# Optimization experiments

Hardware: AMD Instinct MI355X
Metric: run time of the kernel (lower is better)

## Reference

```python
import jax, jax.numpy as jnp
import numpy as np

B, T, E, H = 8, 2048, 256, 8
D = E // H  # head_size = 32
EPS = 1e-5  # torch LayerNorm default


def _layernorm(x, g, b):
    m = jnp.mean(x, axis=-1, keepdims=True)
    v = jnp.var(x, axis=-1, keepdims=True)
    return (x - m) / jnp.sqrt(v + EPS) * g + b


def setup_inputs() -> dict:
    key = jax.random.key(0)
    ks = jax.random.split(key, 9)
    s = lambda k, shape, fan: (jax.random.normal(k, shape, jnp.float32) / np.sqrt(fan)).astype(jnp.float32)
    return {
        "x": jax.random.normal(ks[0], (B, T, E), jnp.float32),
        "wq": s(ks[1], (H, E, D), E),
        "wk": s(ks[2], (H, E, D), E),
        "wv": s(ks[3], (H, E, D), E),
        "w_lin": s(ks[4], (E, E), E),
        "b_lin": jnp.zeros((E,), jnp.float32),
        "g1": jnp.ones((E,), jnp.float32),
        "beta1": jnp.zeros((E,), jnp.float32),
        "g2": jnp.ones((E,), jnp.float32),
        "beta2": jnp.zeros((E,), jnp.float32),
        "w_f1": s(ks[5], (E, 4 * E), E),
        "b_f1": jnp.zeros((4 * E,), jnp.float32),
        "w_f2": s(ks[6], (4 * E, E), 4 * E),
        "b_f2": jnp.zeros((E,), jnp.float32),
    }


def reference(x, wq, wk, wv, w_lin, b_lin, g1, beta1, g2, beta2, w_f1, b_f1, w_f2, b_f2):
    b, t, e = x.shape
    xn = _layernorm(x, g1, beta1)  # norm1
    # all heads at once: (B,T,E) x (H,E,D) -> (B,H,T,D)
    q = jnp.einsum('bte,hed->bhtd', xn, wq)
    k = jnp.einsum('bte,hed->bhtd', xn, wk)
    v = jnp.einsum('bte,hed->bhtd', xn, wv)
    # scale uses C = embedding_size (as in source, not head_size)
    scores = jnp.einsum('bhtd,bhsd->bhts', q, k) * (e ** -0.5)
    mask = jnp.tril(jnp.ones((t, t), bool))  # (query t, key s)
    scores = jnp.where(mask[None, None, :, :], scores, -jnp.inf)
    # source applies softmax over dim=1 of (B,T,T) = the QUERY axis -> axis 2 of bhts
    attn = jax.nn.softmax(scores, axis=2)
    heads = jnp.einsum('bhts,bhsd->bhtd', attn, v)
    heads = heads.transpose(0, 2, 1, 3).reshape(b, t, e)  # concat over heads
    xh = xn + heads  # residual around attention
    xl = xh @ w_lin + b_lin  # projection (dropout is identity at eval)
    x2 = _layernorm(xl, g2, beta2)  # norm2
    ff = jax.nn.relu(x2 @ w_f1 + b_f1) @ w_f2 + b_f2  # FFN (dropout identity)
    return x2 + ff
```

## Files before the change

### kernel.cpp

```cpp
#include <hip/hip_runtime.h>
#include <math.h>

#define TT 2048
#define TE 256
#define NTOK 16384
#define QSCALE (0.0625f * 1.44269504088896f)

typedef short  bf16x8 __attribute__((ext_vector_type(8)));
typedef float  f32x4  __attribute__((ext_vector_type(4)));
typedef float  f32x16 __attribute__((ext_vector_type(16)));
typedef unsigned short u16x4 __attribute__((ext_vector_type(4)));
typedef unsigned short u16x8 __attribute__((ext_vector_type(8)));

__device__ __forceinline__ unsigned short f2b(float f) {
    union { float f; unsigned int u; } v; v.f = f;
    unsigned int r = v.u + 0x7FFF + ((v.u >> 16) & 1);
    return (unsigned short)(r >> 16);
}
__device__ __forceinline__ float b2f(unsigned short u) {
    union { unsigned int i; float f; } v; v.i = ((unsigned int)u) << 16;
    return v.f;
}
#if __has_builtin(__builtin_amdgcn_cvt_pk_bf16_f32)
__device__ __forceinline__ unsigned int pk_bf16(float a, float b) {
    typedef __bf16 bf2 __attribute__((ext_vector_type(2)));
    union { bf2 v; unsigned int u; } u;
    u.v = __builtin_amdgcn_cvt_pk_bf16_f32(a, b);
    return u.u;
}
#else
__device__ __forceinline__ unsigned int pk_bf16(float a, float b) {
    return (unsigned int)f2b(a) | ((unsigned int)f2b(b) << 16);
}
#endif
#if __has_builtin(__builtin_amdgcn_exp2f)
#define FEXP2(x) __builtin_amdgcn_exp2f(x)
#else
#define FEXP2(x) __expf(0.69314718056f * (x))
#endif
__device__ __forceinline__ void pswap(unsigned &a, unsigned &b) {
#if __has_builtin(__builtin_amdgcn_permlane32_swap)
    auto r = __builtin_amdgcn_permlane32_swap(a, b, false, false);
    a = r[0]; b = r[1];
#else
    asm("v_permlane32_swap_b32 %0, %1" : "+v"(a), "+v"(b));
#endif
}
__device__ __forceinline__ bf16x8 ld8(const unsigned short* p) {
    return *(const bf16x8*)p;
}
__device__ __forceinline__ void gl_lds16(const unsigned short* g, unsigned short* l) {
    __builtin_amdgcn_global_load_lds(
        (const __attribute__((address_space(1))) unsigned int*)(uintptr_t)g,
        (__attribute__((address_space(3))) unsigned int*)(uintptr_t)l,
        16, 0, 0);
}
#define MFMA16(a, b, c) __builtin_amdgcn_mfma_f32_16x16x32_bf16((a), (b), (c), 0, 0, 0)
#define MFMA32(a, b, c) __builtin_amdgcn_mfma_f32_32x32x16_bf16((a), (b), (c), 0, 0, 0)
#define SETPRIO(n) __builtin_amdgcn_s_setprio(n)


__device__ __forceinline__ void soft_pv(const f32x16 st, bf16x8 vv0, bf16x8 vv1,
                                        bool diag, int hi, int l31, f32x16& acc) {
    unsigned Wd[8];
    if (diag) {
#pragma unroll
        for (int j = 0; j < 8; ++j) {
            int r0 = 2 * j;
            int s0 = (r0 & 3) + 8 * (r0 >> 2) + 4 * hi;
            float e0 = (s0 <= l31)     ? FEXP2(st[r0])     : 0.f;
            float e1 = (s0 + 1 <= l31) ? FEXP2(st[r0 + 1]) : 0.f;
            Wd[j] = pk_bf16(e0, e1);
        }
    } else {
#pragma unroll
        for (int j = 0; j < 8; ++j)
            Wd[j] = pk_bf16(FEXP2(st[2 * j]), FEXP2(st[2 * j + 1]));
    }
    pswap(Wd[0], Wd[2]); pswap(Wd[1], Wd[3]);
    pswap(Wd[4], Wd[6]); pswap(Wd[5], Wd[7]);
    union { unsigned u4[4]; bf16x8 v; } pa0, pa1;
    pa0.u4[0] = Wd[0]; pa0.u4[1] = Wd[1]; pa0.u4[2] = Wd[2]; pa0.u4[3] = Wd[3];
    pa1.u4[0] = Wd[4]; pa1.u4[1] = Wd[5]; pa1.u4[2] = Wd[6]; pa1.u4[3] = Wd[7];
    SETPRIO(1);
    acc = MFMA32(pa0.v, vv0, acc);
    acc = MFMA32(pa1.v, vv1, acc);
    SETPRIO(0);
}

__device__ __forceinline__ void accum_exp(const f32x16 st, bool diag,
                                          int hi, int l31, float* acc) {
    if (diag) {
#pragma unroll
        for (int r = 0; r < 16; ++r) {
            int s_local = (r & 3) + 8 * (r >> 2) + 4 * hi;
            acc[r] += (l31 >= s_local) ? FEXP2(st[r]) : 0.f;
        }
    } else {
#pragma unroll
        for (int r = 0; r < 16; ++r) acc[r] += FEXP2(st[r]);
    }
}

__global__ __launch_bounds__(256) void prep(const float* __restrict__ wq,
                                            const float* __restrict__ wk,
                                            const float* __restrict__ wv,
                                            const float* __restrict__ w_lin,
                                            const float* __restrict__ w_f1,
                                            const float* __restrict__ w_f2,
                                            unsigned short* __restrict__ Wqkv,
                                            unsigned short* __restrict__ Wlin,
                                            unsigned short* __restrict__ Wf1,
                                            unsigned short* __restrict__ Wf2,
                                            const float* __restrict__ X,
                                            const float* __restrict__ g,
                                            const float* __restrict__ bta,
                                            unsigned short* __restrict__ Yb) {
    int bid = blockIdx.x;
    if (bid >= 240) {
        int row = (bid - 240) * 4 + (threadIdx.x >> 6);
        int lane = threadIdx.x & 63;
        const float4 v = *(const float4*)&X[(size_t)row * TE + lane * 4];
        float s = v.x + v.y + v.z + v.w;
        float s2 = v.x * v.x + v.y * v.y + v.z * v.z + v.w * v.w;
#pragma unroll
        for (int off = 1; off <= 32; off <<= 1) {
            s  += __shfl_xor(s,  off, 64);
            s2 += __shfl_xor(s2, off, 64);
        }
        float mean = s * (1.0f / TE);
        float var = s2 * (1.0f / TE) - mean * mean;
        float rstd = rsqrtf(var + 1e-5f);
        const float4 gg = *(const float4*)&g[lane * 4];
        const float4 bb = *(const float4*)&bta[lane * 4];
        u16x4 ob = { f2b((v.x - mean) * rstd * gg.x + bb.x),
                     f2b((v.y - mean) * rstd * gg.y + bb.y),
                     f2b((v.z - mean) * rstd * gg.z + bb.z),
                     f2b((v.w - mean) * rstd * gg.w + bb.w) };
        *(u16x4*)&Yb[(size_t)row * TE + lane * 4] = ob;
        return;
    }
    __shared__ unsigned short Tt[64][65];
    int t = threadIdx.x;
    if (bid < 96) {
        int which = bid / 32, h = (bid >> 2) & 7, kt = bid & 3;
        const float* src = ((which == 0) ? wq : (which == 1) ? wk : wv)
                           + (size_t)h * 256 * 32;
        int d = t & 31, kr = t >> 5;
#pragma unroll
        for (int r = 0; r < 8; ++r) {
            int kl = kr * 8 + r;
            Tt[kl][d] = f2b(src[(size_t)(kt * 64 + kl) * 32 + d]);
        }
        __syncthreads();
        int kl = t & 63, dr = t >> 6;
#pragma unroll
        for (int r = 0; r < 8; ++r) {
            int dl = dr * 8 + r;
            Wqkv[(size_t)(which * 256 + h * 32 + dl) * 256 + kt * 64 + kl] = Tt[kl][dl];
        }
        return;
    }
    const float* src; unsigned short* dst; int ldn, ldk, kt, nt;
    if (bid < 112)      { int b2 = bid - 96;  src = w_lin; dst = Wlin; ldn = 256;  ldk = 256;  kt = b2 & 3;  nt = b2 >> 2; }
    else if (bid < 176) { int b3 = bid - 112; src = w_f1;  dst = Wf1;  ldn = 1024; ldk = 256;  kt = b3 >> 4; nt = b3 & 15; }
    else                { int b4 = bid - 176; src = w_f2;  dst = Wf2;  ldn = 256;  ldk = 1024; kt = b4 >> 2; nt = b4 & 3; }
    int n = t & 63, kr = t >> 6;
#pragma unroll
    for (int r = 0; r < 16; ++r) {
        int kl = kr * 16 + r;
        Tt[kl][n] = f2b(src[(size_t)(kt * 64 + kl) * ldn + nt * 64 + n]);
    }
    __syncthreads();
    int klane = t & 63, nr = t >> 6;
#pragma unroll
    for (int r = 0; r < 16; ++r) {
        int nl = nr * 16 + r;
        dst[(size_t)(nt * 64 + nl) * ldk + kt * 64 + klane] = Tt[klane][nl];
    }
}

__global__ __launch_bounds__(256) void ln2_red(const float* __restrict__ Pp,
                                               const float* __restrict__ bias,
                                               const float* __restrict__ g,
                                               const float* __restrict__ bta,
                                               unsigned short* __restrict__ Yb) {
    int row = blockIdx.x * 4 + (threadIdx.x >> 6);
    int lane = threadIdx.x & 63;
    size_t base = (size_t)row * TE + lane * 4;
    const float4 p0 = *(const float4*)&Pp[base];
    const float4 bl = *(const float4*)&bias[lane * 4];
    float4 v;
    v.x = p0.x + bl.x; v.y = p0.y + bl.y;
    v.z = p0.z + bl.z; v.w = p0.w + bl.w;
    float s = v.x + v.y + v.z + v.w;
    float s2 = v.x * v.x + v.y * v.y + v.z * v.z + v.w * v.w;
#pragma unroll
    for (int off = 1; off <= 32; off <<= 1) {
        s  += __shfl_xor(s,  off, 64);
        s2 += __shfl_xor(s2, off, 64);
    }
    float mean = s * (1.0f / TE);
    float var = s2 * (1.0f / TE) - mean * mean;
    float rstd = rsqrtf(var + 1e-5f);
    const float4 gg = *(const float4*)&g[lane * 4];
    const float4 bb = *(const float4*)&bta[lane * 4];
    u16x4 ob = { f2b((v.x - mean) * rstd * gg.x + bb.x),
                 f2b((v.y - mean) * rstd * gg.y + bb.y),
                 f2b((v.z - mean) * rstd * gg.z + bb.z),
                 f2b((v.w - mean) * rstd * gg.w + bb.w) };
    *(u16x4*)&Yb[base] = ob;
}

template<int KS>
__global__ __launch_bounds__(256) void gemm_lds(const unsigned short* __restrict__ A,
                                                int lda,
                                                const unsigned short* __restrict__ Bt,
                                                int ldb,
                                                const float* __restrict__ bias,
                                                const unsigned short* __restrict__ resid,
                                                float* __restrict__ outF,
                                                unsigned short* __restrict__ outB,
                                                int N, int relu) {
    __shared__ unsigned short LDSb[3 * 2048 + 3 * 4096];
    unsigned short* Al = LDSb;
    unsigned short* Bl = LDSb + 3 * 2048;
    int tid = threadIdx.x;
    int w = tid >> 6, lane = tid & 63, q = lane >> 4, col = lane & 15;
    int wm = w & 1, wn = w >> 1;
    int m0 = blockIdx.x * 64;
    int n0 = blockIdx.y * 128;
    f32x4 acc[2][4] = {};
    int srow = lane >> 2;
    int skq  = ((lane & 3) ^ ((srow >> 1) & 3)) * 8;
    const unsigned short* Ag0 = A  + (size_t)(m0 + w * 16 + srow) * lda + skq;
    const unsigned short* Bg0 = Bt + (size_t)(n0 + w * 32 + srow) * ldb + skq;
    const unsigned short* Bg1 = Bg0 + (size_t)16 * ldb;
    int rq = (q ^ ((col >> 1) & 3)) * 8;
#define G_STAGE(bf, kk) do { \
        gl_lds16(Ag0 + (kk), &Al[(bf) * 2048 + (w * 16) * 32]); \
        gl_lds16(Bg0 + (kk), &Bl[(bf) * 4096 + (w * 32) * 32]); \
        gl_lds16(Bg1 + (kk), &Bl[(bf) * 4096 + (w * 32 + 16) * 32]); \
    } while (0)
    G_STAGE(0, 0);
    G_STAGE(1, 32);
#pragma unroll
    for (int k0 = 0; k0 < KS; k0 += 32) {
        const int jb = (k0 >> 5) % 3;
        if (k0 + 32 < KS) { asm volatile("s_waitcnt vmcnt(3)" ::: "memory"); }
        else              { asm volatile("s_waitcnt vmcnt(0)" ::: "memory"); }
        __builtin_amdgcn_s_barrier();
        if (k0 + 64 < KS) G_STAGE((jb + 2) % 3, k0 + 64);
        bf16x8 a[2], b[4];
#pragma unroll
        for (int i = 0; i < 2; ++i)
            a[i] = ld8(&Al[jb * 2048 + (wm * 32 + i * 16 + col) * 32 + rq]);
#pragma unroll
        for (int j = 0; j < 4; ++j)
            b[j] = ld8(&Bl[jb * 4096 + (wn * 64 + j * 16 + col) * 32 + rq]);
#pragma unroll
        for (int i = 0; i < 2; ++i)
#pragma unroll
            for (int j = 0; j < 4; ++j)
                acc[i][j] = MFMA16(a[i], b[j], acc[i][j]);
        __builtin_amdgcn_sched_barrier(0);
    }
#undef G_STAGE
    float* Cb = (float*)LDSb;
    const int CLD = 132;
#pragma unroll
    for (int i = 0; i < 2; ++i) {
        __syncthreads();
#pragma unroll
        for (int j = 0; j < 4; ++j)
#pragma unroll
            for (int r = 0; r < 4; ++r)
                Cb[(wm * 16 + q * 4 + r) * CLD + wn * 64 + j * 16 + col] = acc[i][j][r];
        __syncthreads();
        int row = tid >> 3;
        int seg = (tid & 7) * 16;
        int mloc = (row & 15) + i * 16 + (row >> 4) * 32;
        int m = m0 + mloc;
        int n = n0 + seg;
        float vbuf[16];
#pragma unroll
        for (int u = 0; u < 16; ++u) vbuf[u] = Cb[row * CLD + seg + u];
        if (bias) {
#pragma unroll
            for (int u4 = 0; u4 < 4; ++u4) {
                float4 bb = *(const float4*)&bias[n + u4 * 4];
                vbuf[u4 * 4 + 0] += bb.x; vbuf[u4 * 4 + 1] += bb.y;
                vbuf[u4 * 4 + 2] += bb.z; vbuf[u4 * 4 + 3] += bb.w;
            }
        }
        if (resid) {
            u16x8 r0 = *(const u16x8*)&resid[(size_t)m * N + n];
            u16x8 r1 = *(const u16x8*)&resid[(size_t)m * N + n + 8];
#pragma unroll
            for (int u = 0; u < 8; ++u) {
                vbuf[u]     += b2f(r0[u]);
                vbuf[8 + u] += b2f(r1[u]);
            }
        }
        if (relu) {
#pragma unroll
            for (int u = 0; u < 16; ++u) vbuf[u] = fmaxf(vbuf[u], 0.f);
        }
        if (outF) {
#pragma unroll
            for (int u = 0; u < 16; u += 4)
                *(float4*)&outF[(size_t)m * N + n + u] = *(const float4*)&vbuf[u];
        }
        if (outB) {
            u16x8 o0, o1;
#pragma unroll
            for (int u = 0; u < 8; ++u) { o0[u] = f2b(vbuf[u]); o1[u] = f2b(vbuf[8 + u]); }
            *(u16x8*)&outB[(size_t)m * N + n] = o0;
            *(u16x8*)&outB[(size_t)m * N + n + 8] = o1;
        }
    }
}

__global__ __launch_bounds__(256) void gemm_qkv(const unsigned short* __restrict__ A,
                                                const unsigned short* __restrict__ Bt,
                                                unsigned short* __restrict__ Qd,
                                                unsigned short* __restrict__ Kd,
                                                unsigned short* __restrict__ Vc) {
    const int K = 256;
    __shared__ unsigned short LDSb[3 * 2048 + 3 * 4096];
    unsigned short* Al = LDSb;
    unsigned short* Bl = LDSb + 3 * 2048;
    int tid = threadIdx.x;
    int w = tid >> 6, lane = tid & 63, q = lane >> 4, col = lane & 15;
    int wm = w & 1, wn = w >> 1;
    int m0 = blockIdx.x * 64;
    int n0 = blockIdx.y * 128;
    f32x4 acc[2][4] = {};
    int srow = lane >> 2;
    int skq  = ((lane & 3) ^ ((srow >> 1) & 3)) * 8;
    const unsigned short* Ag0 = A  + (size_t)(m0 + w * 16 + srow) * K + skq;
    const unsigned short* Bg0 = Bt + (size_t)(n0 + w * 32 + srow) * K + skq;
    const unsigned short* Bg1 = Bg0 + (size_t)16 * K;
    int rq = (q ^ ((col >> 1) & 3)) * 8;
#define G_STAGE(bf, kk) do { \
        gl_lds16(Ag0 + (kk), &Al[(bf) * 2048 + (w * 16) * 32]); \
        gl_lds16(Bg0 + (kk), &Bl[(bf) * 4096 + (w * 32) * 32]); \
        gl_lds16(Bg1 + (kk), &Bl[(bf) * 4096 + (w * 32 + 16) * 32]); \
    } while (0)
    G_STAGE(0, 0);
    G_STAGE(1, 32);
#pragma unroll
    for (int k0 = 0; k0 < K; k0 += 32) {
        const int jb = (k0 >> 5) % 3;
        if (k0 + 32 < K) { asm volatile("s_waitcnt vmcnt(3)" ::: "memory"); }
        else             { asm volatile("s_waitcnt vmcnt(0)" ::: "memory"); }
        __builtin_amdgcn_s_barrier();
        if (k0 + 64 < K) G_STAGE((jb + 2) % 3, k0 + 64);
        bf16x8 a[2], b[4];
#pragma unroll
        for (int i = 0; i < 2; ++i)
            a[i] = ld8(&Al[jb * 2048 + (wm * 32 + i * 16 + col) * 32 + rq]);
#pragma unroll
        for (int j = 0; j < 4; ++j)
            b[j] = ld8(&Bl[jb * 4096 + (wn * 64 + j * 16 + col) * 32 + rq]);
#pragma unroll
        for (int i = 0; i < 2; ++i)
#pragma unroll
            for (int j = 0; j < 4; ++j)
                acc[i][j] = MFMA16(a[i], b[j], acc[i][j]);
        __builtin_amdgcn_sched_barrier(0);
    }
#undef G_STAGE
#pragma unroll
    for (int i = 0; i < 2; ++i)
#pragma unroll
    for (int j = 0; j < 4; ++j) {
        int n = n0 + wn * 64 + j * 16 + col;
        int which = n >> 8, h = (n >> 5) & 7, d = n & 31;
        int m = m0 + wm * 32 + i * 16 + q * 4;
        int b = m >> 11, t = m & 2047;
        int bh = b * 8 + h;
        if (which == 0) {
            size_t qb = ((size_t)(bh * 2 + (d >> 4)) * TT + t) * 16 + (d & 15);
#pragma unroll
            for (int r = 0; r < 4; ++r)
                Qd[qb + r * 16] = f2b(acc[i][j][r] * QSCALE);
        } else if (which == 1) {
            size_t kb = ((size_t)(bh * 2 + (d >> 4)) * TT + t) * 16 + (d & 15);
#pragma unroll
            for (int r = 0; r < 4; ++r)
                Kd[kb + r * 16] = f2b(acc[i][j][r]);
        } else {
            uint2 pv;
            pv.x = pk_bf16(acc[i][j][0], acc[i][j][1]);
            pv.y = pk_bf16(acc[i][j][2], acc[i][j][3]);
            *(uint2*)&Vc[(((size_t)bh * 256 + (t >> 3)) * 32 + d) * 8 + (t & 7)] = pv;
        }
    }
}

__global__ __launch_bounds__(256, 2) void attn_cols(const unsigned short* __restrict__ Qd,
                                                    const unsigned short* __restrict__ Kd,
                                                    unsigned short* __restrict__ Vc) {
    __shared__ float Lb[4][32];
    __shared__ float Linv[32];
    int tid = threadIdx.x;
    int w = tid >> 6, lane = tid & 63, hi = lane >> 5, l31 = lane & 31;
    int bh = blockIdx.x;
    int stile = blockIdx.y;
    const unsigned short* Qb = Qd + ((size_t)bh * 2 * TT + l31) * 16 + hi * 8;
    const unsigned short* Kb = Kd + ((size_t)bh * 2 * TT + l31) * 16 + hi * 8;
    const f32x16 z16 = {};
    int sbase = stile * 32;
    bf16x8 a0 = ld8(Kb + (size_t)sbase * 16);
    bf16x8 a1 = ld8(Kb + ((size_t)TT + sbase) * 16);
    float acc[16] = {};
    int c = stile + w;
    bool diagP = (w == 0);
    bf16x8 qP0, qP1, qQ0, qQ1;
    if (c < 64) {
        qP0 = ld8(Qb + (size_t)(c * 32) * 16);
        qP1 = ld8(Qb + ((size_t)TT + c * 32) * 16);
    }
    if (c + 4 < 64) {
        qQ0 = ld8(Qb + (size_t)((c + 4) * 32) * 16);
        qQ1 = ld8(Qb + ((size_t)TT + (c + 4) * 32) * 16);
    }
    while (c + 8 < 64) {
        SETPRIO(1);
        f32x16 stP = MFMA32(a0, qP0, z16); stP = MFMA32(a1, qP1, stP);
        SETPRIO(0);
        qP0 = ld8(Qb + (size_t)((c + 8) * 32) * 16);
        qP1 = ld8(Qb + ((size_t)TT + (c + 8) * 32) * 16);
        SETPRIO(1);
        f32x16 stQ = MFMA32(a0, qQ0, z16); stQ = MFMA32(a1, qQ1, stQ);
        SETPRIO(0);
        accum_exp(stP, diagP, hi, l31, acc); diagP = false;
        if (c + 12 < 64) {
            qQ0 = ld8(Qb + (size_t)((c + 12) * 32) * 16);
            qQ1 = ld8(Qb + ((size_t)TT + (c + 12) * 32) * 16);
        }
        accum_exp(stQ, false, hi, l31, acc);
        c += 8;
    }
    if (c < 64) {
        f32x16 stP = MFMA32(a0, qP0, z16); stP = MFMA32(a1, qP1, stP);
        accum_exp(stP, diagP, hi, l31, acc);
    }
    if (c + 4 < 64) {
        f32x16 stQ = MFMA32(a0, qQ0, z16); stQ = MFMA32(a1, qQ1, stQ);
        accum_exp(stQ, false, hi, l31, acc);
    }
#pragma unroll
    for (int off = 1; off <= 16; off <<= 1)
#pragma unroll
        for (int r = 0; r < 16; ++r) acc[r] += __shfl_xor(acc[r], off, 64);
    if (l31 == 0) {
#pragma unroll
        for (int r = 0; r < 16; ++r) {
            int s_local = (r & 3) + 8 * (r >> 2) + 4 * hi;
            Lb[w][s_local] = acc[r];
        }
    }
    __syncthreads();
    if (tid < 32)
        Linv[tid] = 1.0f / (Lb[0][tid] + Lb[1][tid] + Lb[2][tid] + Lb[3][tid]);
    __syncthreads();
    if (tid < 128) {
        int sbl = tid >> 5;
        int d = tid & 31;
        size_t base = (((size_t)bh * 256 + stile * 4 + sbl) * 32 + d) * 8;
        u16x8 v = *(const u16x8*)&Vc[base];
        u16x8 o;
#pragma unroll
        for (int e = 0; e < 8; ++e) o[e] = f2b(b2f(v[e]) * Linv[sbl * 8 + e]);
        *(u16x8*)&Vc[base] = o;
    }
}

__global__ __launch_bounds__(256, 2) void attn_out(const unsigned short* __restrict__ Qd,
                                                   const unsigned short* __restrict__ Kd,
                                                   const unsigned short* __restrict__ Vc,
                                                   const unsigned short* __restrict__ xnb,
                                                   unsigned short* __restrict__ xh_bf) {
    __shared__ float Ob[4][16][36];
    int tid = threadIdx.x;
    int w = tid >> 6, lane = tid & 63, hi = lane >> 5, l31 = lane & 31;
    int bh = blockIdx.x, b = bh >> 3, h = bh & 7;
    int tt = blockIdx.y;
    const unsigned short* Kb = Kd + ((size_t)bh * 2 * TT + l31) * 16 + hi * 8;
    const unsigned short* Vb = Vc + (size_t)bh * 65536 + hi * 256 + l31 * 8;
    const unsigned short* Qbase = Qd + ((size_t)bh * 2 * TT + l31) * 16 + hi * 8;
    const f32x16 z16 = {};

    int tbase = tt * 32;
    bf16x8 q0 = ld8(Qbase + (size_t)tbase * 16);
    bf16x8 q1 = ld8(Qbase + ((size_t)TT + tbase) * 16);
    f32x16 acc = z16;

    int c = w;
    bf16x8 kP0, kP1, vP0, vP1, kQ0, kQ1, vQ0, vQ1;
    if (c <= tt) {
        kP0 = ld8(Kb + (size_t)c * 512);
        kP1 = ld8(Kb + (size_t)TT * 16 + (size_t)c * 512);
        vP0 = ld8(Vb + (size_t)c * 1024);
        vP1 = ld8(Vb + (size_t)c * 1024 + 512);
    }
    if (c + 4 <= tt) {
        kQ0 = ld8(Kb + (size_t)(c + 4) * 512);
        kQ1 = ld8(Kb + (size_t)TT * 16 + (size_t)(c + 4) * 512);
        vQ0 = ld8(Vb + (size_t)(c + 4) * 1024);
        vQ1 = ld8(Vb + (size_t)(c + 4) * 1024 + 512);
    }
    while (c + 8 <= tt) {
        SETPRIO(1);
        f32x16 stP = MFMA32(kP0, q0, z16); stP = MFMA32(kP1, q1, stP);
        SETPRIO(0);
        kP0 = ld8(Kb + (size_t)(c + 8) * 512);
        kP1 = ld8(Kb + (size_t)TT * 16 + (size_t)(c + 8) * 512);
        SETPRIO(1);
        f32x16 stQ = MFMA32(kQ0, q0, z16); stQ = MFMA32(kQ1, q1, stQ);
        SETPRIO(0);
        soft_pv(stP, vP0, vP1, false, hi, l31, acc);
        vP0 = ld8(Vb + (size_t)(c + 8) * 1024);
        vP1 = ld8(Vb + (size_t)(c + 8) * 1024 + 512);
        if (c + 12 <= tt) {
            kQ0 = ld8(Kb + (size_t)(c + 12) * 512);
            kQ1 = ld8(Kb + (size_t)TT * 16 + (size_t)(c + 12) * 512);
        }
        soft_pv(stQ, vQ0, vQ1, false, hi, l31, acc);
        if (c + 12 <= tt) {
            vQ0 = ld8(Vb + (size_t)(c + 12) * 1024);
            vQ1 = ld8(Vb + (size_t)(c + 12) * 1024 + 512);
        }
        c += 8;
    }
    if (c <= tt) {
        f32x16 stP = MFMA32(kP0, q0, z16); stP = MFMA32(kP1, q1, stP);
        soft_pv(stP, vP0, vP1, c == tt, hi, l31, acc);
    }
    if (c + 4 <= tt) {
        f32x16 stQ = MFMA32(kQ0, q0, z16); stQ = MFMA32(kQ1, q1, stQ);
        soft_pv(stQ, vQ0, vQ1, c + 4 == tt, hi, l31, acc);
    }

#pragma unroll
    for (int half = 0; half < 2; ++half) {
#pragma unroll
        for (int rr = 0; rr < 8; ++rr) {
            int r = half * 8 + rr;
            int t16 = (r & 3) + 8 * ((r >> 2) & 1) + 4 * hi;
            Ob[w][t16][l31] = acc[r];
        }
        __syncthreads();
        if (tid < 128) {
            int row = tid >> 3;
            int c4 = (tid & 7) * 4;
            float4 s0 = *(const float4*)&Ob[0][row][c4];
            float4 s1 = *(const float4*)&Ob[1][row][c4];
            float4 s2 = *(const float4*)&Ob[2][row][c4];
            float4 s3 = *(const float4*)&Ob[3][row][c4];
            size_t base = ((size_t)(b * TT) + tbase + half * 16 + row) * TE
                          + h * 32 + c4;
            u16x4 xv = *(const u16x4*)&xnb[base];
            u16x4 ob = { f2b(s0.x + s1.x + s2.x + s3.x + b2f(xv[0])),
                         f2b(s0.y + s1.y + s2.y + s3.y + b2f(xv[1])),
                         f2b(s0.z + s1.z + s2.z + s3.z + b2f(xv[2])),
                         f2b(s0.w + s1.w + s2.w + s3.w + b2f(xv[3])) };
            *(u16x4*)&xh_bf[base] = ob;
        }
        __syncthreads();
    }
}

extern "C" void kernel_launch(void* const* d_in, const int* in_sizes, int n_in,
                              void* d_out, int out_size, void* d_ws, size_t ws_size,
                              hipStream_t stream) {
    (void)in_sizes; (void)n_in; (void)out_size; (void)ws_size;
    const float* x     = (const float*)d_in[0];
    const float* wq    = (const float*)d_in[1];
    const float* wk    = (const float*)d_in[2];
    const float* wv    = (const float*)d_in[3];
    const float* w_lin = (const float*)d_in[4];
    const float* b_lin = (const float*)d_in[5];
    const float* g1    = (const float*)d_in[6];
    const float* beta1 = (const float*)d_in[7];
    const float* g2    = (const float*)d_in[8];
    const float* beta2 = (const float*)d_in[9];
    const float* w_f1  = (const float*)d_in[10];
    const float* b_f1  = (const float*)d_in[11];
    const float* w_f2  = (const float*)d_in[12];
    const float* b_f2  = (const float*)d_in[13];
    float* out = (float*)d_out;

    char* ws = (char*)d_ws;
    unsigned short* Wqkv_t = (unsigned short*)(ws + 0);
    unsigned short* Wlin_t = (unsigned short*)(ws + 393216);
    unsigned short* Wf1_t  = (unsigned short*)(ws + 524288);
    unsigned short* Wf2_t  = (unsigned short*)(ws + 1048576);
    unsigned short* xn_bf  = (unsigned short*)(ws + 2097152);
    unsigned short* Qbf    = (unsigned short*)(ws + 10485760);
    unsigned short* Kbf    = (unsigned short*)(ws + 18874368);
    unsigned short* Vt     = (unsigned short*)(ws + 27262976);
    unsigned short* xh_bf  = (unsigned short*)(ws + 35651584);
    float*          Pp     = (float*)(ws + 44040192);
    unsigned short* x2_bf  = xn_bf;
    unsigned short* h_bf   = Qbf;

    prep<<<4336, 256, 0, stream>>>(wq, wk, wv, w_lin, w_f1, w_f2,
                                   Wqkv_t, Wlin_t, Wf1_t, Wf2_t,
                                   x, g1, beta1, xn_bf);
    gemm_qkv<<<dim3(256, 6), 256, 0, stream>>>(xn_bf, Wqkv_t, Qbf, Kbf, Vt);
    attn_cols<<<dim3(64, 64), 256, 0, stream>>>(Qbf, Kbf, Vt);
    attn_out<<<dim3(64, 64), 256, 0, stream>>>(Qbf, Kbf, Vt, xn_bf, xh_bf);
    gemm_lds<256><<<dim3(256, 2), 256, 0, stream>>>(xh_bf, 256, Wlin_t, 256,
                                                    nullptr, nullptr, Pp, nullptr, 256, 0);
    ln2_red<<<4096, 256, 0, stream>>>(Pp, b_lin, g2, beta2, x2_bf);
    gemm_lds<256><<<dim3(256, 8), 256, 0, stream>>>(x2_bf, 256, Wf1_t, 256,
                                                    b_f1, nullptr, nullptr, h_bf, 1024, 1);
    gemm_lds<1024><<<dim3(256, 2), 256, 0, stream>>>(h_bf, 1024, Wf2_t, 1024,
                                                     b_f2, x2_bf, out, nullptr, 256, 0);
}
```

Measured before the change: 222.4 us.

## Give each wave its own attention tile instead of splitting keys across waves

Both attention kernels now assign each of the four waves its own 32-row tile (tile = blockIdx.y + 16*w) and let it walk the full causal range alone. Previously four waves split one tile's chunks and reduced through shared memory with block barriers. The cross-wave reduction and __syncthreads are gone, the grid shrinks to 64x16 blocks, and launch bounds rise to 4 blocks per CU. Pairing tiles y and y+16, y+32, y+48 in one block balances the causal triangle's work somewhat, but waves within a block still finish at different times, which risks idle waves and tail imbalance.

```diff
diff --git a/kernel.cpp b/kernel.cpp
--- a/kernel.cpp
+++ b/kernel.cpp
@@ -399,15 +399,14 @@
     }
 }
 
-__global__ __launch_bounds__(256, 2) void attn_cols(const unsigned short* __restrict__ Qd,
+__global__ __launch_bounds__(256, 4) void attn_cols(const unsigned short* __restrict__ Qd,
                                                     const unsigned short* __restrict__ Kd,
                                                     unsigned short* __restrict__ Vc) {
-    __shared__ float Lb[4][32];
-    __shared__ float Linv[32];
+    __shared__ float Lw[4][32];
     int tid = threadIdx.x;
     int w = tid >> 6, lane = tid & 63, hi = lane >> 5, l31 = lane & 31;
     int bh = blockIdx.x;
-    int stile = blockIdx.y;
+    int stile = blockIdx.y + 16 * w;
     const unsigned short* Qb = Qd + ((size_t)bh * 2 * TT + l31) * 16 + hi * 8;
     const unsigned short* Kb = Kd + ((size_t)bh * 2 * TT + l31) * 16 + hi * 8;
     const f32x16 z16 = {};
@@ -415,39 +414,37 @@
     bf16x8 a0 = ld8(Kb + (size_t)sbase * 16);
     bf16x8 a1 = ld8(Kb + ((size_t)TT + sbase) * 16);
     float acc[16] = {};
-    int c = stile + w;
-    bool diagP = (w == 0);
+    int c = stile;
+    bool diagP = true;
     bf16x8 qP0, qP1, qQ0, qQ1;
-    if (c < 64) {
-        qP0 = ld8(Qb + (size_t)(c * 32) * 16);
-        qP1 = ld8(Qb + ((size_t)TT + c * 32) * 16);
-    }
-    if (c + 4 < 64) {
-        qQ0 = ld8(Qb + (size_t)((c + 4) * 32) * 16);
-        qQ1 = ld8(Qb + ((size_t)TT + (c + 4) * 32) * 16);
-    }
-    while (c + 8 < 64) {
+    qP0 = ld8(Qb + (size_t)(c * 32) * 16);
+    qP1 = ld8(Qb + ((size_t)TT + c * 32) * 16);
+    if (c + 1 < 64) {
+        qQ0 = ld8(Qb + (size_t)((c + 1) * 32) * 16);
+        qQ1 = ld8(Qb + ((size_t)TT + (c + 1) * 32) * 16);
+    }
+    while (c + 2 < 64) {
         SETPRIO(1);
         f32x16 stP = MFMA32(a0, qP0, z16); stP = MFMA32(a1, qP1, stP);
         SETPRIO(0);
-        qP0 = ld8(Qb + (size_t)((c + 8) * 32) * 16);
-        qP1 = ld8(Qb + ((size_t)TT + (c + 8) * 32) * 16);
+        qP0 = ld8(Qb + (size_t)((c + 2) * 32) * 16);
+        qP1 = ld8(Qb + ((size_t)TT + (c + 2) * 32) * 16);
         SETPRIO(1);
         f32x16 stQ = MFMA32(a0, qQ0, z16); stQ = MFMA32(a1, qQ1, stQ);
         SETPRIO(0);
         accum_exp(stP, diagP, hi, l31, acc); diagP = false;
-        if (c + 12 < 64) {
-            qQ0 = ld8(Qb + (size_t)((c + 12) * 32) * 16);
-            qQ1 = ld8(Qb + ((size_t)TT + (c + 12) * 32) * 16);
+        if (c + 3 < 64) {
+            qQ0 = ld8(Qb + (size_t)((c + 3) * 32) * 16);
+            qQ1 = ld8(Qb + ((size_t)TT + (c + 3) * 32) * 16);
         }
         accum_exp(stQ, false, hi, l31, acc);
-        c += 8;
+        c += 2;
     }
     if (c < 64) {
         f32x16 stP = MFMA32(a0, qP0, z16); stP = MFMA32(a1, qP1, stP);
         accum_exp(stP, diagP, hi, l31, acc);
     }
-    if (c + 4 < 64) {
+    if (c + 1 < 64) {
         f32x16 stQ = MFMA32(a0, qQ0, z16); stQ = MFMA32(a1, qQ1, stQ);
         accum_exp(stQ, false, hi, l31, acc);
     }
@@ -459,35 +456,38 @@
 #pragma unroll
         for (int r = 0; r < 16; ++r) {
             int s_local = (r & 3) + 8 * (r >> 2) + 4 * hi;
-            Lb[w][s_local] = acc[r];
-        }
-    }
-    __syncthreads();
-    if (tid < 32)
-        Linv[tid] = 1.0f / (Lb[0][tid] + Lb[1][tid] + Lb[2][tid] + Lb[3][tid]);
-    __syncthreads();
-    if (tid < 128) {
-        int sbl = tid >> 5;
-        int d = tid & 31;
+            Lw[w][s_local] = acc[r];
+        }
+    }
+    if (lane < 32)
+        Lw[w][lane] = 1.0f / Lw[w][lane];
+#pragma unroll
+    for (int rep = 0; rep < 2; ++rep) {
+        int rr = lane + 64 * rep;
+        int sbl = rr >> 5, d = rr & 31;
         size_t base = (((size_t)bh * 256 + stile * 4 + sbl) * 32 + d) * 8;
         u16x8 v = *(const u16x8*)&Vc[base];
+        const float4 i0 = *(const float4*)&Lw[w][sbl * 8];
+        const float4 i1 = *(const float4*)&Lw[w][sbl * 8 + 4];
         u16x8 o;
-#pragma unroll
-        for (int e = 0; e < 8; ++e) o[e] = f2b(b2f(v[e]) * Linv[sbl * 8 + e]);
+        o[0] = f2b(b2f(v[0]) * i0.x); o[1] = f2b(b2f(v[1]) * i0.y);
+        o[2] = f2b(b2f(v[2]) * i0.z); o[3] = f2b(b2f(v[3]) * i0.w);
+        o[4] = f2b(b2f(v[4]) * i1.x); o[5] = f2b(b2f(v[5]) * i1.y);
+        o[6] = f2b(b2f(v[6]) * i1.z); o[7] = f2b(b2f(v[7]) * i1.w);
         *(u16x8*)&Vc[base] = o;
     }
 }
 
-__global__ __launch_bounds__(256, 2) void attn_out(const unsigned short* __restrict__ Qd,
+__global__ __launch_bounds__(256, 4) void attn_out(const unsigned short* __restrict__ Qd,
                                                    const unsigned short* __restrict__ Kd,
                                                    const unsigned short* __restrict__ Vc,
                                                    const unsigned short* __restrict__ xnb,
                                                    unsigned short* __restrict__ xh_bf) {
-    __shared__ float Ob[4][16][36];
+    __shared__ float Ob[4][32][33];
     int tid = threadIdx.x;
     int w = tid >> 6, lane = tid & 63, hi = lane >> 5, l31 = lane & 31;
     int bh = blockIdx.x, b = bh >> 3, h = bh & 7;
-    int tt = blockIdx.y;
+    int tt = blockIdx.y + 16 * w;
     const unsigned short* Kb = Kd + ((size_t)bh * 2 * TT + l31) * 16 + hi * 8;
     const unsigned short* Vb = Vc + (size_t)bh * 65536 + hi * 256 + l31 * 8;
     const unsigned short* Qbase = Qd + ((size_t)bh * 2 * TT + l31) * 16 + hi * 8;
@@ -498,79 +498,75 @@
     bf16x8 q1 = ld8(Qbase + ((size_t)TT + tbase) * 16);
     f32x16 acc = z16;
 
-    int c = w;
+    int c = 0;
     bf16x8 kP0, kP1, vP0, vP1, kQ0, kQ1, vQ0, vQ1;
-    if (c <= tt) {
-        kP0 = ld8(Kb + (size_t)c * 512);
-        kP1 = ld8(Kb + (size_t)TT * 16 + (size_t)c * 512);
-        vP0 = ld8(Vb + (size_t)c * 1024);
-        vP1 = ld8(Vb + (size_t)c * 1024 + 512);
-    }
-    if (c + 4 <= tt) {
-        kQ0 = ld8(Kb + (size_t)(c + 4) * 512);
-        kQ1 = ld8(Kb + (size_t)TT * 16 + (size_t)(c + 4) * 512);
-        vQ0 = ld8(Vb + (size_t)(c + 4) * 1024);
-        vQ1 = ld8(Vb + (size_t)(c + 4) * 1024 + 512);
-    }
-    while (c + 8 <= tt) {
+    kP0 = ld8(Kb);
+    kP1 = ld8(Kb + (size_t)TT * 16);
+    vP0 = ld8(Vb);
+    vP1 = ld8(Vb + 512);
+    if (1 <= tt) {
+        kQ0 = ld8(Kb + 512);
+        kQ1 = ld8(Kb + (size_t)TT * 16 + 512);
+        vQ0 = ld8(Vb + 1024);
+        vQ1 = ld8(Vb + 1024 + 512);
+    }
+    while (c + 2 <= tt) {
         SETPRIO(1);
         f32x16 stP = MFMA32(kP0, q0, z16); stP = MFMA32(kP1, q1, stP);
         SETPRIO(0);
-        kP0 = ld8(Kb + (size_t)(c + 8) * 512);
-        kP1 = ld8(Kb + (size_t)TT * 16 + (size_t)(c + 8) * 512);
+        kP0 = ld8(Kb + (size_t)(c + 2) * 512);
+        kP1 = ld8(Kb + (size_t)TT * 16 + (size_t)(c + 2) * 512);
         SETPRIO(1);
         f32x16 stQ = MFMA32(kQ0, q0, z16); stQ = MFMA32(kQ1, q1, stQ);
         SETPRIO(0);
         soft_pv(stP, vP0, vP1, false, hi, l31, acc);
-        vP0 = ld8(Vb + (size_t)(c + 8) * 1024);
-        vP1 = ld8(Vb + (size_t)(c + 8) * 1024 + 512);
-        if (c + 12 <= tt) {
-            kQ0 = ld8(Kb + (size_t)(c + 12) * 512);
-            kQ1 = ld8(Kb + (size_t)TT * 16 + (size_t)(c + 12) * 512);
+        vP0 = ld8(Vb + (size_t)(c + 2) * 1024);
+        vP1 = ld8(Vb + (size_t)(c + 2) * 1024 + 512);
+        if (c + 3 <= tt) {
+            kQ0 = ld8(Kb + (size_t)(c + 3) * 512);
+            kQ1 = ld8(Kb + (size_t)TT * 16 + (size_t)(c + 3) * 512);
         }
         soft_pv(stQ, vQ0, vQ1, false, hi, l31, acc);
-        if (c + 12 <= tt) {
-            vQ0 = ld8(Vb + (size_t)(c + 12) * 1024);
-            vQ1 = ld8(Vb + (size_t)(c + 12) * 1024 + 512);
-        }
-        c += 8;
+        if (c + 3 <= tt) {
+            vQ0 = ld8(Vb + (size_t)(c + 3) * 1024);
+            vQ1 = ld8(Vb + (size_t)(c + 3) * 1024 + 512);
+        }
+        c += 2;
     }
     if (c <= tt) {
         f32x16 stP = MFMA32(kP0, q0, z16); stP = MFMA32(kP1, q1, stP);
         soft_pv(stP, vP0, vP1, c == tt, hi, l31, acc);
     }
-    if (c + 4 <= tt) {
+    if (c + 1 <= tt) {
         f32x16 stQ = MFMA32(kQ0, q0, z16); stQ = MFMA32(kQ1, q1, stQ);
-        soft_pv(stQ, vQ0, vQ1, c + 4 == tt, hi, l31, acc);
-    }
-
-#pragma unroll
-    for (int half = 0; half < 2; ++half) {
-#pragma unroll
-        for (int rr = 0; rr < 8; ++rr) {
-            int r = half * 8 + rr;
-            int t16 = (r & 3) + 8 * ((r >> 2) & 1) + 4 * hi;
-            Ob[w][t16][l31] = acc[r];
-        }
-        __syncthreads();
-        if (tid < 128) {
-            int row = tid >> 3;
-            int c4 = (tid & 7) * 4;
-            float4 s0 = *(const float4*)&Ob[0][row][c4];
-            float4 s1 = *(const float4*)&Ob[1][row][c4];
-            float4 s2 = *(const float4*)&Ob[2][row][c4];
-            float4 s3 = *(const float4*)&Ob[3][row][c4];
-            size_t base = ((size_t)(b * TT) + tbase + half * 16 + row) * TE
-                          + h * 32 + c4;
-            u16x4 xv = *(const u16x4*)&xnb[base];
-            u16x4 ob = { f2b(s0.x + s1.x + s2.x + s3.x + b2f(xv[0])),
-                         f2b(s0.y + s1.y + s2.y + s3.y + b2f(xv[1])),
-                         f2b(s0.z + s1.z + s2.z + s3.z + b2f(xv[2])),
-                         f2b(s0.w + s1.w + s2.w + s3.w + b2f(xv[3])) };
-            *(u16x4*)&xh_bf[base] = ob;
-        }
-        __syncthreads();
-    }
+        soft_pv(stQ, vQ0, vQ1, c + 1 == tt, hi, l31, acc);
+    }
+
+#pragma unroll
+    for (int r = 0; r < 16; ++r) {
+        int t = (r & 3) + 8 * (r >> 2) + 4 * hi;
+        Ob[w][t][l31] = acc[r];
+    }
+    int row = lane >> 1;
+    int half = lane & 1;
+    float4 s0 = *(const float4*)&Ob[w][row][half * 16 + 0];
+    float4 s1 = *(const float4*)&Ob[w][row][half * 16 + 4];
+    float4 s2 = *(const float4*)&Ob[w][row][half * 16 + 8];
+    float4 s3 = *(const float4*)&Ob[w][row][half * 16 + 12];
+    size_t base = ((size_t)(b * TT) + tbase + row) * TE + h * 32 + half * 16;
+    u16x8 xv0 = *(const u16x8*)&xnb[base];
+    u16x8 xv1 = *(const u16x8*)&xnb[base + 8];
+    u16x8 o0, o1;
+    o0[0] = f2b(s0.x + b2f(xv0[0])); o0[1] = f2b(s0.y + b2f(xv0[1]));
+    o0[2] = f2b(s0.z + b2f(xv0[2])); o0[3] = f2b(s0.w + b2f(xv0[3]));
+    o0[4] = f2b(s1.x + b2f(xv0[4])); o0[5] = f2b(s1.y + b2f(xv0[5]));
+    o0[6] = f2b(s1.z + b2f(xv0[6])); o0[7] = f2b(s1.w + b2f(xv0[7]));
+    o1[0] = f2b(s2.x + b2f(xv1[0])); o1[1] = f2b(s2.y + b2f(xv1[1]));
+    o1[2] = f2b(s2.z + b2f(xv1[2])); o1[3] = f2b(s2.w + b2f(xv1[3]));
+    o1[4] = f2b(s3.x + b2f(xv1[4])); o1[5] = f2b(s3.y + b2f(xv1[5]));
+    o1[6] = f2b(s3.z + b2f(xv1[6])); o1[7] = f2b(s3.w + b2f(xv1[7]));
+    *(u16x8*)&xh_bf[base] = o0;
+    *(u16x8*)&xh_bf[base + 8] = o1;
 }
 
 extern "C" void kernel_launch(void* const* d_in, const int* in_sizes, int n_in,
@@ -611,8 +607,8 @@
                                    Wqkv_t, Wlin_t, Wf1_t, Wf2_t,
                                    x, g1, beta1, xn_bf);
     gemm_qkv<<<dim3(256, 6), 256, 0, stream>>>(xn_bf, Wqkv_t, Qbf, Kbf, Vt);
-    attn_cols<<<dim3(64, 64), 256, 0, stream>>>(Qbf, Kbf, Vt);
-    attn_out<<<dim3(64, 64), 256, 0, stream>>>(Qbf, Kbf, Vt, xn_bf, xh_bf);
+    attn_cols<<<dim3(64, 16), 256, 0, stream>>>(Qbf, Kbf, Vt);
+    attn_out<<<dim3(64, 16), 256, 0, stream>>>(Qbf, Kbf, Vt, xn_bf, xh_bf);
     gemm_lds<256><<<dim3(256, 2), 256, 0, stream>>>(xh_bf, 256, Wlin_t, 256,
                                                     nullptr, nullptr, Pp, nullptr, 256, 0);
     ln2_red<<<4096, 256, 0, stream>>>(Pp, b_lin, g2, beta2, x2_bf);
```

Result: no change. 222.5 us (+0.1%).
